# Kernel optimization log

Measured on AMD Instinct MI355X. Metric: run time of the kernel, lower is better.

## Reference

```python
import jax, jax.numpy as jnp
import numpy as np

B, L = 8, 2048
D_MAJOR, D_MINOR = 1024, 512
K_REL = 64            # max_relative_distance
R = 2 * K_REL + 1     # number of relative-position buckets


def setup_inputs() -> dict:
    key = jax.random.key(0)
    ks = jax.random.split(key, 10)
    s_in = 0.02
    return {
        "X_major": jax.random.normal(ks[0], (B, L, D_MAJOR), dtype=jnp.float32),
        "X_minor": jax.random.normal(ks[1], (B, L, D_MINOR), dtype=jnp.float32),
        "Wq": jax.random.normal(ks[2], (D_MAJOR, D_MINOR), dtype=jnp.float32) * s_in,
        "Wk": jax.random.normal(ks[3], (D_MINOR, D_MINOR), dtype=jnp.float32) * s_in,
        "Wv": jax.random.normal(ks[4], (D_MINOR, D_MINOR), dtype=jnp.float32) * s_in,
        "aK": jax.random.normal(ks[5], (R, D_MINOR), dtype=jnp.float32) * s_in,  # rel-pos key embeddings
        "aV": jax.random.normal(ks[6], (R, D_MINOR), dtype=jnp.float32) * s_in,  # rel-pos value embeddings
        "ln_gamma": jnp.ones((D_MINOR,), dtype=jnp.float32),
        "ln_beta": jnp.zeros((D_MINOR,), dtype=jnp.float32),
    }


def _layernorm(x, gamma, beta, eps=1e-5):
    mu = jnp.mean(x, axis=-1, keepdims=True)
    var = jnp.mean(jnp.square(x - mu), axis=-1, keepdims=True)
    return (x - mu) * jax.lax.rsqrt(var + eps) * gamma + beta


def reference(X_major, X_minor, Wq, Wk, Wv, aK, aV, ln_gamma, ln_beta):
    # Projections (Shaw et al. relation-aware attention)
    q = X_major @ Wq                      # [B, L, D]
    k = X_minor @ Wk                      # [B, L, D]
    v = X_minor @ Wv                      # [B, L, D]

    # Relative-distance bucket index: clip(j - i, -K, K) + K  -> [L, L]
    pos = jnp.arange(L)
    rel_idx = jnp.clip(pos[None, :] - pos[:, None], -K_REL, K_REL) + K_REL

    # Content scores + relative-position key bias
    scores = jnp.einsum("bqd,bkd->bqk", q, k)                 # [B, L, L]
    rel_scores = jnp.einsum("bqd,rd->bqr", q, aK)             # [B, L, R]
    scores = scores + jnp.take_along_axis(
        rel_scores, jnp.broadcast_to(rel_idx[None], (B, L, L)), axis=2)
    scores = scores / jnp.sqrt(jnp.asarray(D_MINOR, scores.dtype))

    attn = jax.nn.softmax(scores, axis=-1)                    # [B, L, L]
    # attention dropout is identity at inference

    # Context: attn @ V plus relative-position value contribution
    ctx = jnp.einsum("bqk,bkd->bqd", attn, v)                 # [B, L, D]
    # scatter-add attn mass into relative buckets: rel_attn[b,i,r] = sum_j attn[b,i,j] * [rel_idx[i,j]==r]
    ii = jnp.broadcast_to(pos[:, None], (L, L))
    rel_attn = jnp.zeros((B, L, R), dtype=attn.dtype).at[:, ii, rel_idx].add(attn)
    ctx = ctx + rel_attn @ aV                                 # [B, L, D]

    # Wrapper: dropout (identity at eval) + LayerNorm
    Y = _layernorm(ctx, ln_gamma, ln_beta)
    return Y, attn
```

## Files before the change

kernel.cpp:

```cpp
#include <hip/hip_runtime.h>
#include <math.h>

#define NB   8
#define LL   2048
#define DMAJ 1024
#define DMIN 512
#define RR   129
#define KREL 64

typedef short s16x8 __attribute__((ext_vector_type(8)));
typedef float f32x4 __attribute__((ext_vector_type(4)));

__device__ __forceinline__ unsigned short f2bf(float f) {
    union { float f; unsigned u; } v; v.f = f;
    unsigned r = v.u + 0x7fffu + ((v.u >> 16) & 1u);
    return (unsigned short)(r >> 16);
}

__device__ __forceinline__ float bf2f(unsigned short b) {
    union { unsigned u; float f; } v; v.u = (unsigned)b << 16;
    return v.f;
}

__device__ __forceinline__ void gload_lds16(const void* g, void* l) {
    __builtin_amdgcn_global_load_lds(
        (const __attribute__((address_space(1))) void*)g,
        (__attribute__((address_space(3))) void*)l, 16, 0, 0);
}

template<int EPI>
__global__ __launch_bounds__(256) void mfma_nt(
    const float* __restrict__ A, const unsigned short* __restrict__ B,
    void* __restrict__ Cv,
    int M, int N, int K, int lda, int ldb, int ldc,
    long sA, long sB, long sC,
    const float* __restrict__ relS, long sRel)
{
    __shared__ unsigned short Al[128 * 64];
    __shared__ unsigned short Bl[128 * 64];
    const int tid = threadIdx.x;
    const int lane = tid & 63;
    const int w  = tid >> 6;
    const int wm = w >> 1, wn = w & 1;
    const int fr = lane & 15;
    const int kg = lane >> 4;
    const int m0 = blockIdx.y * 128, n0 = blockIdx.x * 128;
    const int b = blockIdx.z;
    const float* Ab = A + (size_t)b * sA;
    const unsigned short* Bb = B + (size_t)b * sB;

    f32x4 acc[4][4];
#pragma unroll
    for (int i = 0; i < 4; ++i)
#pragma unroll
        for (int j = 0; j < 4; ++j) acc[i][j] = f32x4{0.f, 0.f, 0.f, 0.f};

    for (int k0 = 0; k0 < K; k0 += 64) {
        __syncthreads();
#pragma unroll
        for (int p = 0; p < 4; ++p) {
            int idx = p * 256 + tid;
            int row = idx >> 3;
            int c8  = (idx & 7) * 8;
            gload_lds16(Bb + (size_t)(n0 + row) * ldb + k0 + c8, &Bl[idx * 8]);
        }
#pragma unroll
        for (int p = 0; p < 4; ++p) {
            int idx = p * 256 + tid;
            int row = idx >> 3;
            int c8  = (idx & 7) * 8;
            const float* src = Ab + (size_t)(m0 + row) * lda + k0 + c8;
            float4 f0 = *(const float4*)src;
            float4 f1 = *(const float4*)(src + 4);
            union { unsigned short u[8]; int4 v; } pk;
            pk.u[0] = f2bf(f0.x); pk.u[1] = f2bf(f0.y);
            pk.u[2] = f2bf(f0.z); pk.u[3] = f2bf(f0.w);
            pk.u[4] = f2bf(f1.x); pk.u[5] = f2bf(f1.y);
            pk.u[6] = f2bf(f1.z); pk.u[7] = f2bf(f1.w);
            *(int4*)&Al[idx * 8] = pk.v;
        }
        __syncthreads();
#pragma unroll
        for (int kk = 0; kk < 2; ++kk) {
            s16x8 a[4], bf[4];
#pragma unroll
            for (int mi = 0; mi < 4; ++mi)
                a[mi] = *(const s16x8*)&Al[(wm * 64 + mi * 16 + fr) * 64 + kk * 32 + kg * 8];
#pragma unroll
            for (int ni = 0; ni < 4; ++ni)
                bf[ni] = *(const s16x8*)&Bl[(wn * 64 + ni * 16 + fr) * 64 + kk * 32 + kg * 8];
#pragma unroll
            for (int mi = 0; mi < 4; ++mi)
#pragma unroll
                for (int ni = 0; ni < 4; ++ni)
                    acc[mi][ni] = __builtin_amdgcn_mfma_f32_16x16x32_bf16(
                        a[mi], bf[ni], acc[mi][ni], 0, 0, 0);
        }
    }

    const float scale = 0.044194173824159216f;
#pragma unroll
    for (int mi = 0; mi < 4; ++mi) {
#pragma unroll
        for (int ni = 0; ni < 4; ++ni) {
            int n  = n0 + wn * 64 + ni * 16 + fr;
            int mb = m0 + wm * 64 + mi * 16 + kg * 4;
#pragma unroll
            for (int r = 0; r < 4; ++r) {
                int m = mb + r;
                float v = acc[mi][ni][r];
                if (EPI == 0) {
                    ((float*)Cv)[(size_t)b * sC + (size_t)m * ldc + n] = v;
                } else if (EPI == 1) {
                    ((unsigned short*)Cv)[(size_t)b * sC + (size_t)m * ldc + n] = f2bf(v);
                } else {
                    const unsigned short* rSb = (const unsigned short*)relS + (size_t)b * sRel;
                    int rr = n - m;
                    rr = rr < -KREL ? -KREL : (rr > KREL ? KREL : rr);
                    float bias = bf2f(rSb[(size_t)m * 256 + (rr + KREL)]);
                    ((float*)Cv)[(size_t)b * sC + (size_t)m * ldc + n] = (v + bias) * scale;
                }
            }
        }
    }
}

__global__ __launch_bounds__(256) void tcast_bf16_512(const float* __restrict__ W,
                                                      unsigned short* __restrict__ WT,
                                                      int R) {
    int i = blockIdx.x * 256 + threadIdx.x;
    if (i >= R * 512) return;
    int r = i >> 9, c = i & 511;
    WT[(size_t)c * R + r] = f2bf(W[i]);
}

__global__ __launch_bounds__(256) void transpose_f32_512(const float* __restrict__ W,
                                                         float* __restrict__ WT) {
    int i = blockIdx.x * 256 + threadIdx.x;
    int r = i >> 9, c = i & 511;
    WT[(size_t)c * 512 + r] = W[i];
}

__global__ __launch_bounds__(256) void cast_bf16_vec(const float* __restrict__ X,
                                                     unsigned short* __restrict__ Xb,
                                                     long n8) {
    long i = (long)blockIdx.x * 256 + threadIdx.x;
    if (i >= n8) return;
    float4 f0 = ((const float4*)X)[2 * i];
    float4 f1 = ((const float4*)X)[2 * i + 1];
    union { unsigned short u[8]; int4 v; } pk;
    pk.u[0] = f2bf(f0.x); pk.u[1] = f2bf(f0.y);
    pk.u[2] = f2bf(f0.z); pk.u[3] = f2bf(f0.w);
    pk.u[4] = f2bf(f1.x); pk.u[5] = f2bf(f1.y);
    pk.u[6] = f2bf(f1.z); pk.u[7] = f2bf(f1.w);
    ((int4*)Xb)[i] = pk.v;
}

__global__ __launch_bounds__(256) void pad_aK_kernel(const float* __restrict__ aK,
                                                     unsigned short* __restrict__ out) {
    int i = blockIdx.x * 256 + threadIdx.x;
    int r = i >> 9;
    out[i] = (r < RR) ? f2bf(aK[i]) : (unsigned short)0;
}

__global__ __launch_bounds__(256) void softmax_kernel(float* __restrict__ attn) {
    __shared__ float buf[LL];
    __shared__ float red[4];
    float* p = attn + (size_t)blockIdx.x * LL;
    const int tid = threadIdx.x;
    float m = -1e30f;
#pragma unroll
    for (int t = 0; t < 2; ++t) {
        int j4 = tid + t * 256;
        float4 v = ((const float4*)p)[j4];
        ((float4*)buf)[j4] = v;
        m = fmaxf(m, fmaxf(fmaxf(v.x, v.y), fmaxf(v.z, v.w)));
    }
#pragma unroll
    for (int o = 32; o; o >>= 1) m = fmaxf(m, __shfl_down(m, o, 64));
    if ((tid & 63) == 0) red[tid >> 6] = m;
    __syncthreads();
    m = fmaxf(fmaxf(red[0], red[1]), fmaxf(red[2], red[3]));
    __syncthreads();
    float s = 0.f;
#pragma unroll
    for (int t = 0; t < 2; ++t) {
        int j4 = tid + t * 256;
        float4 v = ((const float4*)buf)[j4];
        v.x = __expf(v.x - m); v.y = __expf(v.y - m);
        v.z = __expf(v.z - m); v.w = __expf(v.w - m);
        ((float4*)buf)[j4] = v;
        s += v.x + v.y + v.z + v.w;
    }
#pragma unroll
    for (int o = 32; o; o >>= 1) s += __shfl_down(s, o, 64);
    if ((tid & 63) == 0) red[tid >> 6] = s;
    __syncthreads();
    s = red[0] + red[1] + red[2] + red[3];
    float inv = 1.f / s;
#pragma unroll
    for (int t = 0; t < 2; ++t) {
        int j4 = tid + t * 256;
        float4 v = ((const float4*)buf)[j4];
        v.x *= inv; v.y *= inv; v.z *= inv; v.w *= inv;
        ((float4*)p)[j4] = v;
    }
}

#define BR 16
__global__ __launch_bounds__(256) void relctx_kernel(const float* __restrict__ attn,
                                                     const float* __restrict__ aV,
                                                     float* __restrict__ ctx) {
    __shared__ float rel[BR][132];
    const int tid = threadIdx.x;
    const int row0 = blockIdx.x * BR;
    const int g  = tid >> 4;
    const int lt = tid & 15;
    {
        const int row = row0 + g;
        const int i = row & (LL - 1);
        const float* arow = attn + (size_t)row * LL;
        float slow = 0.f, shigh = 0.f;
        const int lo = i - KREL, hi = i + KREL;
#pragma unroll 4
        for (int k = 0; k < 32; ++k) {
            int j4 = lt + k * 16;
            float4 v = ((const float4*)arow)[j4];
            int j = j4 * 4;
            slow  += (j     <= lo ? v.x : 0.f) + (j + 1 <= lo ? v.y : 0.f)
                   + (j + 2 <= lo ? v.z : 0.f) + (j + 3 <= lo ? v.w : 0.f);
            shigh += (j     >= hi ? v.x : 0.f) + (j + 1 >= hi ? v.y : 0.f)
                   + (j + 2 >= hi ? v.z : 0.f) + (j + 3 >= hi ? v.w : 0.f);
        }
#pragma unroll
        for (int o = 1; o < 16; o <<= 1) {
            slow  += __shfl_xor(slow, o, 16);
            shigh += __shfl_xor(shigh, o, 16);
        }
        if (lt == 0) { rel[g][0] = slow; rel[g][128] = shigh; }
        for (int r = 1 + lt; r < 128; r += 16) {
            int j = i + r - KREL;
            rel[g][r] = (j >= 0 && j < LL) ? arow[j] : 0.f;
        }
    }
    __syncthreads();

    const int rw0 = (tid >> 6) * 4;
    const int d0 = (tid & 63) * 8;
    float acc[4][8];
#pragma unroll
    for (int a = 0; a < 4; ++a)
#pragma unroll
        for (int d = 0; d < 8; ++d) acc[a][d] = 0.f;

    for (int r = 0; r < RR; ++r) {
        float4 av0 = *(const float4*)&aV[(size_t)r * DMIN + d0];
        float4 av1 = *(const float4*)&aV[(size_t)r * DMIN + d0 + 4];
        float rl[4];
#pragma unroll
        for (int a = 0; a < 4; ++a) rl[a] = rel[rw0 + a][r];
#pragma unroll
        for (int a = 0; a < 4; ++a) {
            acc[a][0] += rl[a] * av0.x; acc[a][1] += rl[a] * av0.y;
            acc[a][2] += rl[a] * av0.z; acc[a][3] += rl[a] * av0.w;
            acc[a][4] += rl[a] * av1.x; acc[a][5] += rl[a] * av1.y;
            acc[a][6] += rl[a] * av1.z; acc[a][7] += rl[a] * av1.w;
        }
    }
#pragma unroll
    for (int a = 0; a < 4; ++a) {
        float* dst = ctx + (size_t)(row0 + rw0 + a) * DMIN + d0;
        float4 c0 = *(float4*)dst;
        float4 c1 = *(float4*)(dst + 4);
        c0.x += acc[a][0]; c0.y += acc[a][1]; c0.z += acc[a][2]; c0.w += acc[a][3];
        c1.x += acc[a][4]; c1.y += acc[a][5]; c1.z += acc[a][6]; c1.w += acc[a][7];
        *(float4*)dst = c0;
        *(float4*)(dst + 4) = c1;
    }
}

__global__ __launch_bounds__(256) void layernorm_kernel(float* __restrict__ Y,
                                                        const float* __restrict__ gamma,
                                                        const float* __restrict__ beta) {
    __shared__ float red[4];
    const int row = blockIdx.x;
    float* p = Y + (size_t)row * DMIN;
    const int tid = threadIdx.x;
    float x0 = p[tid], x1 = p[tid + 256];
    float s = x0 + x1;
#pragma unroll
    for (int o = 32; o; o >>= 1) s += __shfl_down(s, o, 64);
    if ((tid & 63) == 0) red[tid >> 6] = s;
    __syncthreads();
    float mu = (red[0] + red[1] + red[2] + red[3]) * (1.f / 512.f);
    __syncthreads();
    float d0 = x0 - mu, d1 = x1 - mu;
    float v = d0 * d0 + d1 * d1;
#pragma unroll
    for (int o = 32; o; o >>= 1) v += __shfl_down(v, o, 64);
    if ((tid & 63) == 0) red[tid >> 6] = v;
    __syncthreads();
    float var = (red[0] + red[1] + red[2] + red[3]) * (1.f / 512.f);
    float inv = rsqrtf(var + 1e-5f);
    p[tid] = d0 * inv * gamma[tid] + beta[tid];
    p[tid + 256] = d1 * inv * gamma[tid + 256] + beta[tid + 256];
}

extern "C" void kernel_launch(void* const* d_in, const int* in_sizes, int n_in,
                              void* d_out, int out_size, void* d_ws, size_t ws_size,
                              hipStream_t stream) {
    const float* Xmaj  = (const float*)d_in[0];
    const float* Xmin  = (const float*)d_in[1];
    const float* Wq    = (const float*)d_in[2];
    const float* Wk    = (const float*)d_in[3];
    const float* Wv    = (const float*)d_in[4];
    const float* aK    = (const float*)d_in[5];
    const float* aV    = (const float*)d_in[6];
    const float* gamma = (const float*)d_in[7];
    const float* beta  = (const float*)d_in[8];

    float* Y    = (float*)d_out;
    float* attn = Y + (size_t)NB * LL * DMIN;

    float* q = (float*)d_ws;
    unsigned short* relS_bf = (unsigned short*)(q + (size_t)16384 * 512);
    float* WvT = (float*)(relS_bf + (size_t)16384 * 256);
    unsigned short* k_bf    = (unsigned short*)(WvT + 512 * 512);
    unsigned short* vT_bf   = k_bf + (size_t)16384 * 512;
    unsigned short* Xmin_bf = vT_bf + (size_t)512 * 16384;
    unsigned short* WqT_bf  = Xmin_bf + (size_t)16384 * 512;
    unsigned short* WkT_bf  = WqT_bf + (size_t)512 * 1024;
    unsigned short* aK_bf   = WkT_bf + (size_t)512 * 512;

    const int M = NB * LL;
    dim3 blk(256);

    tcast_bf16_512<<<dim3(2048), blk, 0, stream>>>(Wq, WqT_bf, 1024);
    tcast_bf16_512<<<dim3(1024), blk, 0, stream>>>(Wk, WkT_bf, 512);
    transpose_f32_512<<<dim3(1024), blk, 0, stream>>>(Wv, WvT);
    cast_bf16_vec<<<dim3(4096), blk, 0, stream>>>(Xmin, Xmin_bf, (long)M * DMIN / 8);
    pad_aK_kernel<<<dim3(512), blk, 0, stream>>>(aK, aK_bf);

    mfma_nt<0><<<dim3(4, 128, 1), blk, 0, stream>>>(
        Xmaj, WqT_bf, q, M, DMIN, DMAJ, DMAJ, DMAJ, DMIN, 0, 0, 0, nullptr, 0);
    mfma_nt<1><<<dim3(4, 128, 1), blk, 0, stream>>>(
        Xmin, WkT_bf, k_bf, M, DMIN, DMIN, DMIN, DMIN, DMIN, 0, 0, 0, nullptr, 0);
    mfma_nt<1><<<dim3(128, 4, 1), blk, 0, stream>>>(
        WvT, Xmin_bf, vT_bf, DMIN, M, DMIN, DMIN, DMIN, M, 0, 0, 0, nullptr, 0);

    mfma_nt<1><<<dim3(2, 128, 1), blk, 0, stream>>>(
        q, aK_bf, relS_bf, M, 256, DMIN, DMIN, DMIN, 256, 0, 0, 0, nullptr, 0);

    mfma_nt<2><<<dim3(16, 16, NB), blk, 0, stream>>>(
        q, k_bf, attn, LL, LL, DMIN, DMIN, DMIN, LL,
        (long)LL * DMIN, (long)LL * DMIN, (long)LL * LL,
        (const float*)relS_bf, (long)LL * 256);

    softmax_kernel<<<dim3(M), blk, 0, stream>>>(attn);

    mfma_nt<0><<<dim3(4, 16, NB), blk, 0, stream>>>(
        attn, vT_bf, Y, LL, DMIN, LL, LL, M, DMIN,
        (long)LL * LL, (long)LL, (long)LL * DMIN, nullptr, 0);

    relctx_kernel<<<dim3(M / BR), blk, 0, stream>>>(attn, aV, Y);
    layernorm_kernel<<<dim3(M), blk, 0, stream>>>(Y, gamma, beta);
}
```

Measured before the change: 671.2 us.

## Fuse softmax into attn·V GEMM and layernorm into relative-context kernel

Replaces the standalone softmax kernel and the separate attn@V GEMM with one kernel. It first computes per-row max and sum with an online-softmax pass over the raw scores. Then, while staging each K-tile, it normalizes the scores, writes the final attention back to global memory, converts it to bf16 in LDS and runs MFMA against V. Layernorm is also folded into the relative-position context kernel using wave-level shuffle reductions, which removes one full read/write of the output and a launch. The trade-off is a much smaller grid (256 blocks of 512 threads) and an unpipelined tile loop, so occupancy and latency hiding may suffer.

```diff
diff --git a/kernel.cpp b/kernel.cpp
--- a/kernel.cpp
+++ b/kernel.cpp
@@ -125,6 +125,115 @@
     }
 }
 
+__global__ __launch_bounds__(512) void smpv_kernel(
+    float* __restrict__ attn,
+    const unsigned short* __restrict__ vT,
+    float* __restrict__ Y)
+{
+    __shared__ unsigned short Al[64 * 64];
+    __shared__ unsigned short Bl[512 * 64];
+    __shared__ float sm_m[64], sm_il[64];
+    const int tid = threadIdx.x;
+    const int b = blockIdx.z;
+    const int m0 = blockIdx.x * 64;
+    float* abase = attn + (size_t)b * LL * LL;
+
+    {
+        const int r = tid >> 3, l = tid & 7;
+        const float* arow = abase + (size_t)(m0 + r) * LL;
+        float m = -1e30f, s = 0.f;
+        for (int k = 0; k < 64; ++k) {
+            float4 v = ((const float4*)arow)[l + k * 8];
+            float mx = fmaxf(fmaxf(v.x, v.y), fmaxf(v.z, v.w));
+            float nm = fmaxf(m, mx);
+            s = s * __expf(m - nm)
+              + __expf(v.x - nm) + __expf(v.y - nm)
+              + __expf(v.z - nm) + __expf(v.w - nm);
+            m = nm;
+        }
+#pragma unroll
+        for (int o = 1; o < 8; o <<= 1) {
+            float om = __shfl_xor(m, o, 8);
+            float os = __shfl_xor(s, o, 8);
+            float nm = fmaxf(m, om);
+            s = s * __expf(m - nm) + os * __expf(om - nm);
+            m = nm;
+        }
+        if (l == 0) { sm_m[r] = m; sm_il[r] = 1.f / s; }
+    }
+
+    const int lane = tid & 63;
+    const int w  = tid >> 6;
+    const int wm = w >> 2, wn = w & 3;
+    const int fr = lane & 15;
+    const int kg = lane >> 4;
+
+    f32x4 acc[2][8];
+#pragma unroll
+    for (int i = 0; i < 2; ++i)
+#pragma unroll
+        for (int j = 0; j < 8; ++j) acc[i][j] = f32x4{0.f, 0.f, 0.f, 0.f};
+
+    for (int kt = 0; kt < 32; ++kt) {
+        __syncthreads();
+#pragma unroll
+        for (int p = 0; p < 8; ++p) {
+            int idx = p * 512 + tid;
+            int d  = idx >> 3;
+            int c8 = (idx & 7) * 8;
+            gload_lds16(vT + (size_t)d * 16384 + b * LL + kt * 64 + c8, &Bl[idx * 8]);
+        }
+#pragma unroll
+        for (int p = 0; p < 2; ++p) {
+            int idx = p * 512 + tid;
+            int r  = idx >> 4;
+            int c4 = idx & 15;
+            float* src = abase + (size_t)(m0 + r) * LL + kt * 64 + c4 * 4;
+            float4 v = *(const float4*)src;
+            float mm = sm_m[r], il = sm_il[r];
+            v.x = __expf(v.x - mm) * il;
+            v.y = __expf(v.y - mm) * il;
+            v.z = __expf(v.z - mm) * il;
+            v.w = __expf(v.w - mm) * il;
+            *(float4*)src = v;
+            union { unsigned short u[4]; int2 q; } pk;
+            pk.u[0] = f2bf(v.x); pk.u[1] = f2bf(v.y);
+            pk.u[2] = f2bf(v.z); pk.u[3] = f2bf(v.w);
+            *(int2*)&Al[r * 64 + c4 * 4] = pk.q;
+        }
+        __syncthreads();
+#pragma unroll
+        for (int kk = 0; kk < 2; ++kk) {
+            s16x8 a[2], bf[8];
+#pragma unroll
+            for (int mi = 0; mi < 2; ++mi)
+                a[mi] = *(const s16x8*)&Al[(wm * 32 + mi * 16 + fr) * 64 + kk * 32 + kg * 8];
+#pragma unroll
+            for (int ni = 0; ni < 8; ++ni)
+                bf[ni] = *(const s16x8*)&Bl[(wn * 128 + ni * 16 + fr) * 64 + kk * 32 + kg * 8];
+#pragma unroll
+            for (int mi = 0; mi < 2; ++mi)
+#pragma unroll
+                for (int ni = 0; ni < 8; ++ni)
+                    acc[mi][ni] = __builtin_amdgcn_mfma_f32_16x16x32_bf16(
+                        a[mi], bf[ni], acc[mi][ni], 0, 0, 0);
+        }
+    }
+
+#pragma unroll
+    for (int mi = 0; mi < 2; ++mi) {
+#pragma unroll
+        for (int ni = 0; ni < 8; ++ni) {
+            int n = wn * 128 + ni * 16 + fr;
+            int mb = m0 + wm * 32 + mi * 16 + kg * 4;
+#pragma unroll
+            for (int r = 0; r < 4; ++r) {
+                Y[(size_t)(b * LL + mb + r) * DMIN + n] = acc[mi][ni][r];
+            }
+        }
+    }
+}
+
 __global__ __launch_bounds__(256) void tcast_bf16_512(const float* __restrict__ W,
                                                       unsigned short* __restrict__ WT,
                                                       int R) {
@@ -163,54 +272,12 @@
     out[i] = (r < RR) ? f2bf(aK[i]) : (unsigned short)0;
 }
 
-__global__ __launch_bounds__(256) void softmax_kernel(float* __restrict__ attn) {
-    __shared__ float buf[LL];
-    __shared__ float red[4];
-    float* p = attn + (size_t)blockIdx.x * LL;
-    const int tid = threadIdx.x;
-    float m = -1e30f;
-#pragma unroll
-    for (int t = 0; t < 2; ++t) {
-        int j4 = tid + t * 256;
-        float4 v = ((const float4*)p)[j4];
-        ((float4*)buf)[j4] = v;
-        m = fmaxf(m, fmaxf(fmaxf(v.x, v.y), fmaxf(v.z, v.w)));
-    }
-#pragma unroll
-    for (int o = 32; o; o >>= 1) m = fmaxf(m, __shfl_down(m, o, 64));
-    if ((tid & 63) == 0) red[tid >> 6] = m;
-    __syncthreads();
-    m = fmaxf(fmaxf(red[0], red[1]), fmaxf(red[2], red[3]));
-    __syncthreads();
-    float s = 0.f;
-#pragma unroll
-    for (int t = 0; t < 2; ++t) {
-        int j4 = tid + t * 256;
-        float4 v = ((const float4*)buf)[j4];
-        v.x = __expf(v.x - m); v.y = __expf(v.y - m);
-        v.z = __expf(v.z - m); v.w = __expf(v.w - m);
-        ((float4*)buf)[j4] = v;
-        s += v.x + v.y + v.z + v.w;
-    }
-#pragma unroll
-    for (int o = 32; o; o >>= 1) s += __shfl_down(s, o, 64);
-    if ((tid & 63) == 0) red[tid >> 6] = s;
-    __syncthreads();
-    s = red[0] + red[1] + red[2] + red[3];
-    float inv = 1.f / s;
-#pragma unroll
-    for (int t = 0; t < 2; ++t) {
-        int j4 = tid + t * 256;
-        float4 v = ((const float4*)buf)[j4];
-        v.x *= inv; v.y *= inv; v.z *= inv; v.w *= inv;
-        ((float4*)p)[j4] = v;
-    }
-}
-
 #define BR 16
-__global__ __launch_bounds__(256) void relctx_kernel(const float* __restrict__ attn,
-                                                     const float* __restrict__ aV,
-                                                     float* __restrict__ ctx) {
+__global__ __launch_bounds__(256) void relln_kernel(const float* __restrict__ attn,
+                                                    const float* __restrict__ aV,
+                                                    float* __restrict__ ctx,
+                                                    const float* __restrict__ gamma,
+                                                    const float* __restrict__ beta) {
     __shared__ float rel[BR][132];
     const int tid = threadIdx.x;
     const int row0 = blockIdx.x * BR;
@@ -267,43 +334,41 @@
             acc[a][6] += rl[a] * av1.z; acc[a][7] += rl[a] * av1.w;
         }
     }
+
+    float4 g0 = *(const float4*)&gamma[d0];
+    float4 g1 = *(const float4*)&gamma[d0 + 4];
+    float4 b0 = *(const float4*)&beta[d0];
+    float4 b1 = *(const float4*)&beta[d0 + 4];
+
 #pragma unroll
     for (int a = 0; a < 4; ++a) {
         float* dst = ctx + (size_t)(row0 + rw0 + a) * DMIN + d0;
         float4 c0 = *(float4*)dst;
         float4 c1 = *(float4*)(dst + 4);
-        c0.x += acc[a][0]; c0.y += acc[a][1]; c0.z += acc[a][2]; c0.w += acc[a][3];
-        c1.x += acc[a][4]; c1.y += acc[a][5]; c1.z += acc[a][6]; c1.w += acc[a][7];
+        float x[8];
+        x[0] = c0.x + acc[a][0]; x[1] = c0.y + acc[a][1];
+        x[2] = c0.z + acc[a][2]; x[3] = c0.w + acc[a][3];
+        x[4] = c1.x + acc[a][4]; x[5] = c1.y + acc[a][5];
+        x[6] = c1.z + acc[a][6]; x[7] = c1.w + acc[a][7];
+        float s = 0.f;
+#pragma unroll
+        for (int d = 0; d < 8; ++d) s += x[d];
+#pragma unroll
+        for (int o = 32; o; o >>= 1) s += __shfl_xor(s, o, 64);
+        float mu = s * (1.f / 512.f);
+        float v = 0.f;
+#pragma unroll
+        for (int d = 0; d < 8; ++d) { x[d] -= mu; v += x[d] * x[d]; }
+#pragma unroll
+        for (int o = 32; o; o >>= 1) v += __shfl_xor(v, o, 64);
+        float inv = rsqrtf(v * (1.f / 512.f) + 1e-5f);
+        c0.x = x[0] * inv * g0.x + b0.x; c0.y = x[1] * inv * g0.y + b0.y;
+        c0.z = x[2] * inv * g0.z + b0.z; c0.w = x[3] * inv * g0.w + b0.w;
+        c1.x = x[4] * inv * g1.x + b1.x; c1.y = x[5] * inv * g1.y + b1.y;
+        c1.z = x[6] * inv * g1.z + b1.z; c1.w = x[7] * inv * g1.w + b1.w;
         *(float4*)dst = c0;
         *(float4*)(dst + 4) = c1;
     }
-}
-
-__global__ __launch_bounds__(256) void layernorm_kernel(float* __restrict__ Y,
-                                                        const float* __restrict__ gamma,
-                                                        const float* __restrict__ beta) {
-    __shared__ float red[4];
-    const int row = blockIdx.x;
-    float* p = Y + (size_t)row * DMIN;
-    const int tid = threadIdx.x;
-    float x0 = p[tid], x1 = p[tid + 256];
-    float s = x0 + x1;
-#pragma unroll
-    for (int o = 32; o; o >>= 1) s += __shfl_down(s, o, 64);
-    if ((tid & 63) == 0) red[tid >> 6] = s;
-    __syncthreads();
-    float mu = (red[0] + red[1] + red[2] + red[3]) * (1.f / 512.f);
-    __syncthreads();
-    float d0 = x0 - mu, d1 = x1 - mu;
-    float v = d0 * d0 + d1 * d1;
-#pragma unroll
-    for (int o = 32; o; o >>= 1) v += __shfl_down(v, o, 64);
-    if ((tid & 63) == 0) red[tid >> 6] = v;
-    __syncthreads();
-    float var = (red[0] + red[1] + red[2] + red[3]) * (1.f / 512.f);
-    float inv = rsqrtf(var + 1e-5f);
-    p[tid] = d0 * inv * gamma[tid] + beta[tid];
-    p[tid + 256] = d1 * inv * gamma[tid + 256] + beta[tid + 256];
 }
 
 extern "C" void kernel_launch(void* const* d_in, const int* in_sizes, int n_in,
@@ -356,12 +421,7 @@
         (long)LL * DMIN, (long)LL * DMIN, (long)LL * LL,
         (const float*)relS_bf, (long)LL * 256);
 
-    softmax_kernel<<<dim3(M), blk, 0, stream>>>(attn);
-
-    mfma_nt<0><<<dim3(4, 16, NB), blk, 0, stream>>>(
-        attn, vT_bf, Y, LL, DMIN, LL, LL, M, DMIN,
-        (long)LL * LL, (long)LL, (long)LL * DMIN, nullptr, 0);
-
-    relctx_kernel<<<dim3(M / BR), blk, 0, stream>>>(attn, aV, Y);
-    layernorm_kernel<<<dim3(M), blk, 0, stream>>>(Y, gamma, beta);
-}
+    smpv_kernel<<<dim3(32, 1, NB), dim3(512), 0, stream>>>(attn, vT_bf, Y);
+
+    relln_kernel<<<dim3(M / BR), blk, 0, stream>>>(attn, aV, Y, gamma, beta);
+}
```

After: 668.5 us. About the same (-0.4%).
